# Kernel tuning notes

Hardware: AMD Instinct MI355X
Metric: run time of the kernel (lower is better)

Reference implementation:

```python
import jax, jax.numpy as jnp
import numpy as np

B = 8192
D = 512          # hidden_dim
OBS_EMB = 256
COMM = 128
N_ACT = 4
N_LAYERS = 2
D_INNER = 2 * D
D_STATE = 16
DT_RANK = D // 16  # 32
D_CONV = 4
EPS = 1e-5


def _xavier(k, shape):
    s = jnp.sqrt(2.0 / (shape[-2] + shape[-1]))
    return jax.random.normal(k, shape, jnp.float32) * s


def setup_inputs() -> dict:
    ks = jax.random.split(jax.random.key(0), 16)
    p = {}
    p['obs'] = jax.random.normal(ks[0], (B, 75), jnp.float32)
    p['comm_in'] = jax.random.normal(ks[1], (B, COMM), jnp.float32)
    # obs encoder: Conv2d(3->32, k=3, valid) + Linear(288->256)
    p['conv_w'] = jax.random.normal(ks[2], (32, 3, 3, 3), jnp.float32) * jnp.sqrt(2.0 / 27.0)
    p['conv_b'] = jnp.zeros((32,), jnp.float32)
    p['enc_w'] = _xavier(ks[3], (288, OBS_EMB))
    p['enc_b'] = jnp.zeros((OBS_EMB,), jnp.float32)
    p['proj_w'] = _xavier(ks[4], (OBS_EMB + COMM, D))
    p['proj_b'] = jnp.zeros((D,), jnp.float32)
    # Mamba stack params (stacked over layers)
    p['norm_w'] = jnp.ones((N_LAYERS, D), jnp.float32)
    p['in_proj_w'] = _xavier(ks[5], (N_LAYERS, D, 2 * D_INNER))
    p['conv1d_w'] = jax.random.normal(ks[6], (N_LAYERS, D_INNER, D_CONV), jnp.float32) / jnp.sqrt(D_CONV)
    p['conv1d_b'] = jnp.zeros((N_LAYERS, D_INNER), jnp.float32)
    p['x_proj_w'] = _xavier(ks[7], (N_LAYERS, D_INNER, DT_RANK + 2 * D_STATE))
    p['dt_proj_w'] = _xavier(ks[8], (N_LAYERS, DT_RANK, D_INNER))
    p['dt_proj_b'] = jnp.full((N_LAYERS, D_INNER), jnp.log(jnp.expm1(0.01)), jnp.float32)  # dt ~ 0.01
    p['A_log'] = jnp.log(jnp.broadcast_to(jnp.arange(1, D_STATE + 1, dtype=jnp.float32), (N_LAYERS, D_INNER, D_STATE)))
    p['D_param'] = jnp.ones((N_LAYERS, D_INNER), jnp.float32)
    p['out_proj_w'] = _xavier(ks[9], (N_LAYERS, D_INNER, D))
    p['final_norm_w'] = jnp.ones((D,), jnp.float32)
    # output heads
    p['act_w'] = _xavier(ks[10], (D, N_ACT)); p['act_b'] = jnp.zeros((N_ACT,), jnp.float32)
    p['comm_w'] = _xavier(ks[11], (D, COMM)); p['comm_b'] = jnp.zeros((COMM,), jnp.float32)
    p['val_w'] = _xavier(ks[12], (D, 1)); p['val_b'] = jnp.zeros((1,), jnp.float32)
    return p


def _rmsnorm(x, w):
    return x * jax.lax.rsqrt(jnp.mean(x * x, axis=-1, keepdims=True) + EPS) * w


def _mamba_block(u, Wi, cw, cb, Wx, Wdt, bdt, Alog, Dp, Wo):
    # u: (B, L, D) -> (B, L, D)
    Bsz, L, _ = u.shape
    d_inner = Dp.shape[0]
    x, z = jnp.split(u @ Wi, 2, axis=-1)                       # (B,L,di) each
    # causal depthwise conv1d over L
    xt = jnp.pad(jnp.swapaxes(x, 1, 2), ((0, 0), (0, 0), (D_CONV - 1, 0)))
    xc = jax.lax.conv_general_dilated(xt, cw[:, None, :], (1,), 'VALID',
                                      feature_group_count=d_inner,
                                      dimension_numbers=('NCH', 'OIH', 'NCH'))
    x = jax.nn.silu(jnp.swapaxes(xc, 1, 2) + cb)
    x_dbl = x @ Wx                                              # (B,L,dt_rank+2*ns)
    dt = jax.nn.softplus(x_dbl[..., :DT_RANK] @ Wdt + bdt)      # (B,L,di)
    Bm = x_dbl[..., DT_RANK:DT_RANK + D_STATE]                  # (B,L,ns)
    Cm = x_dbl[..., DT_RANK + D_STATE:]                         # (B,L,ns)
    A = -jnp.exp(Alog)                                          # (di,ns)
    dA = jnp.exp(dt[..., None] * A)                             # (B,L,di,ns)
    dBx = dt[..., None] * Bm[:, :, None, :] * x[..., None]      # (B,L,di,ns)

    def step(h, inp):
        dA_t, dBx_t, C_t = inp
        h = dA_t * h + dBx_t
        return h, jnp.einsum('bds,bs->bd', h, C_t)

    h0 = jnp.zeros((Bsz, d_inner, D_STATE), u.dtype)
    _, ys = jax.lax.scan(step, h0, (jnp.swapaxes(dA, 0, 1), jnp.swapaxes(dBx, 0, 1), jnp.swapaxes(Cm, 0, 1)))
    y = jnp.swapaxes(ys, 0, 1) + x * Dp
    return (y * jax.nn.silu(z)) @ Wo


def reference(obs, comm_in, conv_w, conv_b, enc_w, enc_b, proj_w, proj_b,
              norm_w, in_proj_w, conv1d_w, conv1d_b, x_proj_w, dt_proj_w, dt_proj_b,
              A_log, D_param, out_proj_w, final_norm_w,
              act_w, act_b, comm_w, comm_b, val_w, val_b):
    Bsz = obs.shape[0]
    v = obs.reshape(Bsz, 3, 5, 5)
    v = jax.lax.conv_general_dilated(v, conv_w, (1, 1), 'VALID',
                                     dimension_numbers=('NCHW', 'OIHW', 'NCHW'))
    v = jax.nn.relu(v + conv_b[None, :, None, None]).reshape(Bsz, -1)   # (B,288)
    emb = jax.nn.relu(v @ enc_w + enc_b)                                 # (B,256)
    x = jax.nn.relu(jnp.concatenate([emb, comm_in], axis=-1) @ proj_w + proj_b)  # (B,512)
    h = x[:, None, :]                                                    # (B, L=1, D)
    for i in range(norm_w.shape[0]):
        h = h + _mamba_block(_rmsnorm(h, norm_w[i]), in_proj_w[i], conv1d_w[i],
                             conv1d_b[i], x_proj_w[i], dt_proj_w[i], dt_proj_b[i],
                             A_log[i], D_param[i], out_proj_w[i])
    h = _rmsnorm(h, final_norm_w)[:, 0, :]
    action_logits = h @ act_w + act_b
    comm_out = jnp.tanh(h @ comm_w + comm_b)
    value = h @ val_w + val_b
    return action_logits, comm_out, value
```

## Files before the change

### kernel.cpp

```cpp
#include <hip/hip_runtime.h>
#include <math.h>


typedef __bf16 bf16x8 __attribute__((ext_vector_type(8)));
typedef float f32x4 __attribute__((ext_vector_type(4)));
typedef short short8 __attribute__((ext_vector_type(8)));

__device__ __forceinline__ float siluf(float v){ return v / (1.f + __expf(-v)); }
__device__ __forceinline__ float spfast(float v){ return v > 15.f ? v : __logf(1.f + __expf(v)); }
__device__ __forceinline__ float b2f(unsigned short u){ return __uint_as_float(((unsigned)u)<<16); }
__device__ __forceinline__ unsigned short f2b(float f){
  unsigned u = __float_as_uint(f);
  return (unsigned short)((u + 0x7fffu + ((u>>16)&1u)) >> 16);
}
__device__ __forceinline__ void g2l16(const void* g, void* l){
  __builtin_amdgcn_global_load_lds((const __attribute__((address_space(1))) unsigned int*)g,
                                   (__attribute__((address_space(3))) unsigned int*)l, 16, 0, 0);
}

__global__ __launch_bounds__(256) void k_wt_all(
    const float* __restrict__ in_proj_w, const float* __restrict__ out_proj_w,
    const float* __restrict__ x_proj_w,  const float* __restrict__ dt_proj_w,
    const float* __restrict__ enc_w,     const float* __restrict__ proj_w,
    const float* __restrict__ act_w, const float* __restrict__ comm_w, const float* __restrict__ val_w,
    unsigned short* __restrict__ wi_t, unsigned short* __restrict__ wo_t,
    unsigned short* __restrict__ wx_t, unsigned short* __restrict__ wdt_t,
    unsigned short* __restrict__ we_t, unsigned short* __restrict__ wp_t,
    unsigned short* __restrict__ wh_t)
{
  int b = blockIdx.x;
  if (b >= 3536) {
    const int n = b - 3536;
    for (int k = threadIdx.x; k < 512; k += 256) {
      float v;
      if (n < 4)         v = act_w[k*4 + n];
      else if (n < 132)  v = comm_w[k*128 + (n-4)];
      else if (n == 132) v = val_w[k];
      else               v = 0.f;
      wh_t[(size_t)n*512 + k] = f2b(v);
    }
    return;
  }
  const float* Wsrc; unsigned short* Wdst; int Kd, Nd, KP, nkb;
  if (b < 2048) {
    const int L = b >> 10; b &= 1023;
    Wsrc = in_proj_w + (size_t)L*512*2048; Wdst = wi_t + (size_t)L*2048*512;
    Kd = 512; Nd = 2048; KP = 512; nkb = 16;
  } else if (b < 3072) {
    b -= 2048; const int L = b >> 9; b &= 511;
    Wsrc = out_proj_w + (size_t)L*1024*512; Wdst = wo_t + (size_t)L*512*1024;
    Kd = 1024; Nd = 512; KP = 1024; nkb = 32;
  } else if (b < 3200) {
    b -= 3072; const int L = b >> 6; b &= 63;
    Wsrc = x_proj_w + (size_t)L*1024*64; Wdst = wx_t + (size_t)L*64*1024;
    Kd = 1024; Nd = 64; KP = 1024; nkb = 32;
  } else if (b < 3264) {
    b -= 3200; const int L = b >> 5; b &= 31;
    Wsrc = dt_proj_w + (size_t)L*32*1024; Wdst = wdt_t + (size_t)L*1024*32;
    Kd = 32; Nd = 1024; KP = 32; nkb = 1;
  } else if (b < 3344) {
    b -= 3264; Wsrc = enc_w; Wdst = we_t; Kd = 288; Nd = 256; KP = 320; nkb = 10;
  } else {
    b -= 3344; Wsrc = proj_w; Wdst = wp_t; Kd = 384; Nd = 512; KP = 384; nkb = 12;
  }
  __shared__ float s[32][33];
  const int kb = (b % nkb)*32, nb = (b / nkb)*32;
  const int c = threadIdx.x & 31, r = threadIdx.x >> 5;
  #pragma unroll
  for (int i=0;i<32;i+=8) {
    const int k = kb + r + i;
    s[r+i][c] = (k < Kd) ? Wsrc[(size_t)k*Nd + nb + c] : 0.f;
  }
  __syncthreads();
  #pragma unroll
  for (int i=0;i<32;i+=8) Wdst[(size_t)(nb+r+i)*KP + kb + c] = f2b(s[c][r+i]);
}

__global__ __launch_bounds__(256) void k_rms(const float* __restrict__ h,
                                             const float* __restrict__ nw,
                                             unsigned short* __restrict__ u)
{
  const int l = threadIdx.x & 63;
  const size_t row = (size_t)blockIdx.x*4 + (threadIdx.x>>6);
  const float4* hp = (const float4*)(h + row*512) + l*2;
  float4 v0 = hp[0], v1 = hp[1];
  float ss = v0.x*v0.x+v0.y*v0.y+v0.z*v0.z+v0.w*v0.w
           + v1.x*v1.x+v1.y*v1.y+v1.z*v1.z+v1.w*v1.w;
  #pragma unroll
  for (int m=32;m;m>>=1) ss += __shfl_xor(ss, m, 64);
  const float sc = rsqrtf(ss*(1.f/512.f) + 1e-5f);
  const float4* np = (const float4*)nw + l*2;
  float4 w0 = np[0], w1 = np[1];
  short8 o;
  o[0]=(short)f2b(v0.x*sc*w0.x); o[1]=(short)f2b(v0.y*sc*w0.y);
  o[2]=(short)f2b(v0.z*sc*w0.z); o[3]=(short)f2b(v0.w*sc*w0.w);
  o[4]=(short)f2b(v1.x*sc*w1.x); o[5]=(short)f2b(v1.y*sc*w1.y);
  o[6]=(short)f2b(v1.z*sc*w1.z); o[7]=(short)f2b(v1.w*sc*w1.w);
  *(short8*)(u + row*512 + l*8) = o;
}

template<int K>
__device__ __forceinline__ void gemm128(const unsigned short* __restrict__ A,
                                        const unsigned short* __restrict__ Bt,
                                        int r0, int c0,
                                        unsigned short* sA, unsigned short* sB,
                                        f32x4 acc[4][4])
{
  const int tid = threadIdx.x;
  const int l = tid & 63;
  const int wr = (tid>>7)&1, wc = (tid>>6)&1;
  const int rowA = tid>>3, kc8 = (tid&7)*8;
  const unsigned short* gA = A  + (size_t)(r0+rowA)*K + kc8;
  const unsigned short* gB = Bt + (size_t)(c0+rowA)*K + kc8;
  const int aOff = (wr*64 + (l&15))*64 + ((l>>4)*8);
  const int bOff = (wc*64 + (l&15))*64 + ((l>>4)*8);
  for (int kt=0; kt<K; kt+=64) {
    #pragma unroll
    for (int it=0; it<4; ++it) {
      g2l16(gA + (size_t)(it*32)*K + kt, sA + ((it*256+tid)*8));
      g2l16(gB + (size_t)(it*32)*K + kt, sB + ((it*256+tid)*8));
    }
    __syncthreads();
    #pragma unroll
    for (int ks=0; ks<64; ks+=32) {
      bf16x8 af[4], bfm[4];
      #pragma unroll
      for (int m=0;m<4;m++) af[m]  = *(const bf16x8*)(sA + (m*16)*64 + aOff + ks);
      #pragma unroll
      for (int n=0;n<4;n++) bfm[n] = *(const bf16x8*)(sB + (n*16)*64 + bOff + ks);
      #pragma unroll
      for (int m=0;m<4;m++)
        #pragma unroll
        for (int n=0;n<4;n++)
          acc[m][n] = __builtin_amdgcn_mfma_f32_16x16x32_bf16(af[m], bfm[n], acc[m][n], 0, 0, 0);
    }
    __syncthreads();
  }
}

__global__ __launch_bounds__(256) void k_gemm_inproj(
    const unsigned short* __restrict__ A, const unsigned short* __restrict__ Bt,
    const float* __restrict__ cw, const float* __restrict__ cb,
    unsigned short* __restrict__ xs, unsigned short* __restrict__ zs)
{
  __shared__ unsigned short sA[128*64], sB[128*64];
  f32x4 acc[4][4];
  #pragma unroll
  for (int m=0;m<4;m++)
    #pragma unroll
    for (int n=0;n<4;n++) acc[m][n] = (f32x4){0.f,0.f,0.f,0.f};
  const int r0 = blockIdx.x*128, c0 = blockIdx.y*128;
  gemm128<512>(A, Bt, r0, c0, sA, sB, acc);

  const int tid = threadIdx.x, l = tid & 63;
  const int wr = (tid>>7)&1, wc = (tid>>6)&1;
  const int colB = c0 + wc*64 + (l&15);
  const int rowB = r0 + wr*64 + ((l>>4)*4);
  if (c0 < 1024) {
    #pragma unroll
    for (int n=0;n<4;n++){
      const int col = colB + n*16;
      const float cw3 = cw[col*4+3], cbv = cb[col];
      #pragma unroll
      for (int m=0;m<4;m++)
        #pragma unroll
        for (int j=0;j<4;j++){
          const int row = rowB + m*16 + j;
          xs[(size_t)row*1024 + col] = f2b(siluf(fmaf(acc[m][n][j], cw3, cbv)));
        }
    }
  } else {
    #pragma unroll
    for (int n=0;n<4;n++){
      const int col = colB + n*16 - 1024;
      #pragma unroll
      for (int m=0;m<4;m++)
        #pragma unroll
        for (int j=0;j<4;j++){
          const int row = rowB + m*16 + j;
          zs[(size_t)row*1024 + col] = f2b(siluf(acc[m][n][j]));
        }
    }
  }
}

__global__ __launch_bounds__(256) void k_gemm_outproj(
    const unsigned short* __restrict__ A, const unsigned short* __restrict__ Bt,
    float* __restrict__ h)
{
  __shared__ unsigned short sA[128*64], sB[128*64];
  f32x4 acc[4][4];
  #pragma unroll
  for (int m=0;m<4;m++)
    #pragma unroll
    for (int n=0;n<4;n++) acc[m][n] = (f32x4){0.f,0.f,0.f,0.f};
  const int r0 = blockIdx.x*128, c0 = blockIdx.y*128;
  gemm128<1024>(A, Bt, r0, c0, sA, sB, acc);

  const int tid = threadIdx.x, l = tid & 63;
  const int wr = (tid>>7)&1, wc = (tid>>6)&1;
  const int colB = c0 + wc*64 + (l&15);
  const int rowB = r0 + wr*64 + ((l>>4)*4);
  #pragma unroll
  for (int n=0;n<4;n++){
    const int col = colB + n*16;
    #pragma unroll
    for (int m=0;m<4;m++)
      #pragma unroll
      for (int j=0;j<4;j++){
        const int row = rowB + m*16 + j;
        h[(size_t)row*512 + col] += acc[m][n][j];
      }
  }
}

__global__ __launch_bounds__(256) void k_gemm_enc(
    const unsigned short* __restrict__ A, const unsigned short* __restrict__ Bt,
    const float* __restrict__ bias, unsigned short* __restrict__ cat)
{
  __shared__ unsigned short sA[128*64], sB[128*64];
  f32x4 acc[4][4];
  #pragma unroll
  for (int m=0;m<4;m++)
    #pragma unroll
    for (int n=0;n<4;n++) acc[m][n] = (f32x4){0.f,0.f,0.f,0.f};
  const int r0 = blockIdx.x*128, c0 = blockIdx.y*128;
  gemm128<320>(A, Bt, r0, c0, sA, sB, acc);

  const int tid = threadIdx.x, l = tid & 63;
  const int wr = (tid>>7)&1, wc = (tid>>6)&1;
  const int colB = c0 + wc*64 + (l&15);
  const int rowB = r0 + wr*64 + ((l>>4)*4);
  #pragma unroll
  for (int n=0;n<4;n++){
    const int col = colB + n*16;
    const float bv = bias[col];
    #pragma unroll
    for (int m=0;m<4;m++)
      #pragma unroll
      for (int j=0;j<4;j++){
        const size_t row = rowB + m*16 + j;
        cat[row*384 + col] = f2b(fmaxf(acc[m][n][j] + bv, 0.f));
      }
  }
}

__global__ __launch_bounds__(256) void k_gemm_proj(
    const unsigned short* __restrict__ A, const unsigned short* __restrict__ Bt,
    const float* __restrict__ bias, float* __restrict__ h)
{
  __shared__ unsigned short sA[128*64], sB[128*64];
  f32x4 acc[4][4];
  #pragma unroll
  for (int m=0;m<4;m++)
    #pragma unroll
    for (int n=0;n<4;n++) acc[m][n] = (f32x4){0.f,0.f,0.f,0.f};
  const int r0 = blockIdx.x*128, c0 = blockIdx.y*128;
  gemm128<384>(A, Bt, r0, c0, sA, sB, acc);

  const int tid = threadIdx.x, l = tid & 63;
  const int wr = (tid>>7)&1, wc = (tid>>6)&1;
  const int colB = c0 + wc*64 + (l&15);
  const int rowB = r0 + wr*64 + ((l>>4)*4);
  #pragma unroll
  for (int n=0;n<4;n++){
    const int col = colB + n*16;
    const float bv = bias[col];
    #pragma unroll
    for (int m=0;m<4;m++)
      #pragma unroll
      for (int j=0;j<4;j++){
        const size_t row = rowB + m*16 + j;
        h[row*512 + col] = fmaxf(acc[m][n][j] + bv, 0.f);
      }
  }
}

__global__ __launch_bounds__(256) void k_front_prep(
    const float* __restrict__ obs, const float* __restrict__ comm_in,
    const float* __restrict__ conv_w, const float* __restrict__ conv_b,
    unsigned short* __restrict__ v, unsigned short* __restrict__ cat)
{
  __shared__ float s_obs[8][76];
  const int t = threadIdx.x;
  const int r0 = blockIdx.x * 8;

  for (int i = t; i < 8*75; i += 256) s_obs[i/75][i%75] = obs[(size_t)(r0 + i/75)*75 + i%75];
  __syncthreads();

  for (int i = t; i < 8*288; i += 256) {
    int r = i / 288, o = i % 288;
    int c = o / 9, ij = o % 9, oi = ij/3, oj = ij%3;
    float acc = conv_b[c];
    #pragma unroll
    for (int ic=0; ic<3; ic++)
      #pragma unroll
      for (int ki=0; ki<3; ki++)
        #pragma unroll
        for (int kj=0; kj<3; kj++)
          acc = fmaf(s_obs[r][ic*25 + (oi+ki)*5 + (oj+kj)], conv_w[((c*3+ic)*3+ki)*3+kj], acc);
    v[(size_t)(r0+r)*320 + o] = f2b(fmaxf(acc, 0.f));
  }
  v[(size_t)(r0 + (t>>5))*320 + 288 + (t&31)] = 0;
  for (int i = t; i < 8*128; i += 256) {
    int r = i >> 7, c = i & 127;
    cat[(size_t)(r0+r)*384 + 256 + c] = f2b(comm_in[(size_t)(r0+r)*128 + c]);
  }
}

__global__ __launch_bounds__(256) void k_gemm_heads(
    const unsigned short* __restrict__ A, const unsigned short* __restrict__ Bt,
    const float* __restrict__ act_b, const float* __restrict__ comm_b,
    const float* __restrict__ val_b, float* __restrict__ out)
{
  __shared__ unsigned short sA[128*64], sB[128*64];
  f32x4 acc[4][4];
  #pragma unroll
  for (int m=0;m<4;m++)
    #pragma unroll
    for (int n=0;n<4;n++) acc[m][n] = (f32x4){0.f,0.f,0.f,0.f};
  const int r0 = blockIdx.x*128, c0 = blockIdx.y*128;
  gemm128<512>(A, Bt, r0, c0, sA, sB, acc);

  const int tid = threadIdx.x, l = tid & 63;
  const int wr = (tid>>7)&1, wc = (tid>>6)&1;
  const int colB = c0 + wc*64 + (l&15);
  const int rowB = r0 + wr*64 + ((l>>4)*4);
  #pragma unroll
  for (int n=0;n<4;n++){
    const int col = colB + n*16;
    if (col > 132) continue;
    #pragma unroll
    for (int m=0;m<4;m++)
      #pragma unroll
      for (int j=0;j<4;j++){
        const size_t row = rowB + m*16 + j;
        float v = acc[m][n][j];
        if (col < 4)        out[row*4 + col] = v + act_b[col];
        else if (col < 132) out[32768 + row*128 + (col-4)] = tanhf(v + comm_b[col-4]);
        else                out[1081344 + row] = v + val_b[0];
      }
  }
}

__global__ __launch_bounds__(256) void k_xdbl(
    const unsigned short* __restrict__ A, const unsigned short* __restrict__ Bt,
    float* __restrict__ xdbl)
{
  __shared__ unsigned short sA[128*64], sB[64*64];
  f32x4 acc[2][4];
  #pragma unroll
  for (int m=0;m<2;m++)
    #pragma unroll
    for (int n=0;n<4;n++) acc[m][n] = (f32x4){0.f,0.f,0.f,0.f};
  const int tid = threadIdx.x, l = tid & 63, w = tid>>6;
  const int r0 = blockIdx.x*128;
  const int rowA = tid>>3, kc8 = (tid&7)*8;
  const unsigned short* gA = A  + (size_t)(r0+rowA)*1024 + kc8;
  const unsigned short* gB = Bt + (size_t)rowA*1024 + kc8;
  const int aOff = (w*32 + (l&15))*64 + ((l>>4)*8);
  const int bOff = ((l&15))*64 + ((l>>4)*8);
  for (int kt=0; kt<1024; kt+=64) {
    #pragma unroll
    for (int it=0; it<4; ++it) g2l16(gA + (size_t)(it*32)*1024 + kt, sA + (it*256+tid)*8);
    #pragma unroll
    for (int it=0; it<2; ++it) g2l16(gB + (size_t)(it*32)*1024 + kt, sB + (it*256+tid)*8);
    __syncthreads();
    #pragma unroll
    for (int ks=0; ks<64; ks+=32) {
      bf16x8 af[2], bfm[4];
      #pragma unroll
      for (int m=0;m<2;m++) af[m]  = *(const bf16x8*)(sA + (m*16)*64 + aOff + ks);
      #pragma unroll
      for (int n=0;n<4;n++) bfm[n] = *(const bf16x8*)(sB + (n*16)*64 + bOff + ks);
      #pragma unroll
      for (int m=0;m<2;m++)
        #pragma unroll
        for (int n=0;n<4;n++)
          acc[m][n] = __builtin_amdgcn_mfma_f32_16x16x32_bf16(af[m], bfm[n], acc[m][n], 0, 0, 0);
    }
    __syncthreads();
  }
  #pragma unroll
  for (int n=0;n<4;n++){
    const int col = n*16 + (l&15);
    #pragma unroll
    for (int m=0;m<2;m++)
      #pragma unroll
      for (int j=0;j<4;j++){
        const size_t row = r0 + w*32 + m*16 + (l>>4)*4 + j;
        xdbl[row*64 + col] = acc[m][n][j];
      }
  }
}

__global__ __launch_bounds__(256) void k_dtgate(
    unsigned short* __restrict__ xs, const unsigned short* __restrict__ zs,
    const float* __restrict__ xdbl, const unsigned short* __restrict__ Wdt_t,
    const float* __restrict__ bdt, const float* __restrict__ Dp)
{
  __shared__ unsigned short sA[128*32];
  __shared__ unsigned short sB[128*32];
  __shared__ float s_bc[128];
  const int tid = threadIdx.x, l = tid & 63;
  const int r0 = blockIdx.x*128, c0 = blockIdx.y*128;

  {
    const int row = tid >> 1, kh = (tid & 1)*16;
    const float4* p = (const float4*)(xdbl + (size_t)(r0+row)*64 + kh);
    float4 a = p[0], b = p[1], c = p[2], d = p[3];
    short8 o0, o1;
    o0[0]=(short)f2b(a.x); o0[1]=(short)f2b(a.y); o0[2]=(short)f2b(a.z); o0[3]=(short)f2b(a.w);
    o0[4]=(short)f2b(b.x); o0[5]=(short)f2b(b.y); o0[6]=(short)f2b(b.z); o0[7]=(short)f2b(b.w);
    o1[0]=(short)f2b(c.x); o1[1]=(short)f2b(c.y); o1[2]=(short)f2b(c.z); o1[3]=(short)f2b(c.w);
    o1[4]=(short)f2b(d.x); o1[5]=(short)f2b(d.y); o1[6]=(short)f2b(d.z); o1[7]=(short)f2b(d.w);
    *(short8*)(sA + row*32 + kh)     = o0;
    *(short8*)(sA + row*32 + kh + 8) = o1;
  }
  {
    const int nrow = tid >> 1, kh = (tid & 1)*16;
    const short8* wp = (const short8*)(Wdt_t + (size_t)(c0+nrow)*32 + kh);
    *(short8*)(sB + nrow*32 + kh)     = wp[0];
    *(short8*)(sB + nrow*32 + kh + 8) = wp[1];
  }
  if (tid < 128) {
    const float4* q = (const float4*)(xdbl + (size_t)(r0+tid)*64 + 32);
    float4 b0=q[0], b1=q[1], b2=q[2], b3=q[3];
    float4 c0v=q[4], c1=q[5], c2=q[6], c3=q[7];
    float acc = b0.x*c0v.x + b0.y*c0v.y + b0.z*c0v.z + b0.w*c0v.w
              + b1.x*c1.x + b1.y*c1.y + b1.z*c1.z + b1.w*c1.w
              + b2.x*c2.x + b2.y*c2.y + b2.z*c2.z + b2.w*c2.w
              + b3.x*c3.x + b3.y*c3.y + b3.z*c3.z + b3.w*c3.w;
    s_bc[tid] = acc;
  }
  __syncthreads();

  const int wr = (tid>>7)&1, wc = (tid>>6)&1;
  bf16x8 af[4], bfm[4];
  #pragma unroll
  for (int m=0;m<4;m++) af[m]  = *(const bf16x8*)(sA + (wr*64 + m*16 + (l&15))*32 + (l>>4)*8);
  #pragma unroll
  for (int n=0;n<4;n++) bfm[n] = *(const bf16x8*)(sB + (wc*64 + n*16 + (l&15))*32 + (l>>4)*8);
  f32x4 acc[4][4];
  #pragma unroll
  for (int m=0;m<4;m++)
    #pragma unroll
    for (int n=0;n<4;n++)
      acc[m][n] = __builtin_amdgcn_mfma_f32_16x16x32_bf16(af[m], bfm[n], (f32x4){0.f,0.f,0.f,0.f}, 0, 0, 0);

  #pragma unroll
  for (int n=0;n<4;n++){
    const int col = c0 + wc*64 + n*16 + (l&15);
    const float bj = bdt[col], dpj = Dp[col];
    #pragma unroll
    for (int m=0;m<4;m++){
      const int rloc = wr*64 + m*16 + (l>>4)*4;
      #pragma unroll
      for (int j=0;j<4;j++){
        const size_t row = r0 + rloc + j;
        const float dtv = spfast(acc[m][n][j] + bj);
        const float f = fmaf(dtv, s_bc[rloc + j], dpj);
        const float x = b2f(xs[row*1024 + col]);
        const float z = b2f(zs[row*1024 + col]);
        xs[row*1024 + col] = f2b(x * f * z);
      }
    }
  }
}

extern "C" void kernel_launch(void* const* d_in, const int* in_sizes, int n_in,
                              void* d_out, int out_size, void* d_ws, size_t ws_size,
                              hipStream_t stream) {
  const float* obs       = (const float*)d_in[0];
  const float* comm_in   = (const float*)d_in[1];
  const float* conv_w    = (const float*)d_in[2];
  const float* conv_b    = (const float*)d_in[3];
  const float* enc_w     = (const float*)d_in[4];
  const float* enc_b     = (const float*)d_in[5];
  const float* proj_w    = (const float*)d_in[6];
  const float* proj_b    = (const float*)d_in[7];
  const float* norm_w    = (const float*)d_in[8];
  const float* in_proj_w = (const float*)d_in[9];
  const float* conv1d_w  = (const float*)d_in[10];
  const float* conv1d_b  = (const float*)d_in[11];
  const float* x_proj_w  = (const float*)d_in[12];
  const float* dt_proj_w = (const float*)d_in[13];
  const float* dt_proj_b = (const float*)d_in[14];
  const float* D_param   = (const float*)d_in[16];
  const float* out_proj_w= (const float*)d_in[17];
  const float* final_nw  = (const float*)d_in[18];
  const float* act_w     = (const float*)d_in[19];
  const float* act_b     = (const float*)d_in[20];
  const float* comm_w    = (const float*)d_in[21];
  const float* comm_b    = (const float*)d_in[22];
  const float* val_w     = (const float*)d_in[23];
  const float* val_b     = (const float*)d_in[24];
  float* out = (float*)d_out;

  char* W = (char*)d_ws;
  float* h             = (float*)W;
  unsigned short* u_b  = (unsigned short*)(W + (16u<<20));
  unsigned short* xs_b = (unsigned short*)(W + (24u<<20));
  unsigned short* zs_b = (unsigned short*)(W + (40u<<20));
  unsigned short* wi_t = (unsigned short*)(W + (56u<<20));
  unsigned short* wo_t = (unsigned short*)(W + (60u<<20));
  float* xdbl          = (float*)(W + (62u<<20));
  unsigned short* wx_t = (unsigned short*)(W + (64u<<20));
  unsigned short* wdt_t= (unsigned short*)(W + (64u<<20) + (256u<<10));
  unsigned short* wh_t = (unsigned short*)(W + (65u<<20));
  unsigned short* we_t = (unsigned short*)(W + (65u<<20) + (512u<<10));
  unsigned short* wp_t = (unsigned short*)(W + (66u<<20));

  unsigned short* v_b   = xs_b;
  unsigned short* cat_b = zs_b;

  k_wt_all<<<3792,256,0,stream>>>(in_proj_w, out_proj_w, x_proj_w, dt_proj_w,
                                  enc_w, proj_w, act_w, comm_w, val_w,
                                  wi_t, wo_t, wx_t, wdt_t, we_t, wp_t, wh_t);

  k_front_prep<<<1024,256,0,stream>>>(obs, comm_in, conv_w, conv_b, v_b, cat_b);
  k_gemm_enc<<<dim3(64,2),256,0,stream>>>(v_b, we_t, enc_b, cat_b);
  k_gemm_proj<<<dim3(64,4),256,0,stream>>>(cat_b, wp_t, proj_b, h);

  for (int L=0; L<2; L++) {
    k_rms<<<2048,256,0,stream>>>(h, norm_w + L*512, u_b);
    k_gemm_inproj<<<dim3(64,16),256,0,stream>>>(u_b, wi_t + (size_t)L*2048*512,
                                                conv1d_w + L*1024*4, conv1d_b + L*1024, xs_b, zs_b);
    k_xdbl<<<64,256,0,stream>>>(xs_b, wx_t + (size_t)L*64*1024, xdbl);
    k_dtgate<<<dim3(64,8),256,0,stream>>>(xs_b, zs_b, xdbl, wdt_t + (size_t)L*1024*32,
                                          dt_proj_b + L*1024, D_param + L*1024);
    k_gemm_outproj<<<dim3(64,4),256,0,stream>>>(xs_b, wo_t + (size_t)L*512*1024, h);
  }
  k_rms<<<2048,256,0,stream>>>(h, final_nw, u_b);
  k_gemm_heads<<<dim3(64,2),256,0,stream>>>(u_b, wh_t, act_b, comm_b, val_b, out);
}
```

Baseline: 279.4 us.

## Narrow GEMM tiles, split x_proj finer with precomputed dt/BC, merge front prep

The small-N GEMMs (enc, proj, out_proj, heads) move to 128x64 tiles to launch more blocks on the 256-CU device. The x_proj GEMM now runs with 32-row blocks (256 blocks instead of 64) and directly writes bf16 dt inputs and the B·C dot product, so dtgate no longer converts or reduces xdbl. The front-end conv preprocessing is folded into the weight-transpose launch to save one kernel launch. Narrower tiles reduce A-tile reuse and add redundant A loads.

After: 253.7 us. 9.2% less time.

```diff
diff --git a/kernel.cpp b/kernel.cpp
--- a/kernel.cpp
+++ b/kernel.cpp
@@ -5,6 +5,7 @@
 typedef __bf16 bf16x8 __attribute__((ext_vector_type(8)));
 typedef float f32x4 __attribute__((ext_vector_type(4)));
 typedef short short8 __attribute__((ext_vector_type(8)));
+typedef short short4v __attribute__((ext_vector_type(4)));
 
 __device__ __forceinline__ float siluf(float v){ return v / (1.f + __expf(-v)); }
 __device__ __forceinline__ float spfast(float v){ return v > 15.f ? v : __logf(1.f + __expf(v)); }
@@ -23,21 +24,51 @@
     const float* __restrict__ x_proj_w,  const float* __restrict__ dt_proj_w,
     const float* __restrict__ enc_w,     const float* __restrict__ proj_w,
     const float* __restrict__ act_w, const float* __restrict__ comm_w, const float* __restrict__ val_w,
+    const float* __restrict__ obs, const float* __restrict__ comm_in,
+    const float* __restrict__ conv_w, const float* __restrict__ conv_b,
     unsigned short* __restrict__ wi_t, unsigned short* __restrict__ wo_t,
     unsigned short* __restrict__ wx_t, unsigned short* __restrict__ wdt_t,
     unsigned short* __restrict__ we_t, unsigned short* __restrict__ wp_t,
-    unsigned short* __restrict__ wh_t)
+    unsigned short* __restrict__ wh_t,
+    unsigned short* __restrict__ v, unsigned short* __restrict__ cat)
 {
   int b = blockIdx.x;
+  const int t = threadIdx.x;
+
+  if (b >= 3792) {
+    __shared__ float s_obs[8][76];
+    const int r0 = (b - 3792) * 8;
+    for (int i = t; i < 8*75; i += 256) s_obs[i/75][i%75] = obs[(size_t)(r0 + i/75)*75 + i%75];
+    __syncthreads();
+    for (int i = t; i < 8*288; i += 256) {
+      int r = i / 288, o = i % 288;
+      int c = o / 9, ij = o % 9, oi = ij/3, oj = ij%3;
+      float acc = conv_b[c];
+      #pragma unroll
+      for (int ic=0; ic<3; ic++)
+        #pragma unroll
+        for (int ki=0; ki<3; ki++)
+          #pragma unroll
+          for (int kj=0; kj<3; kj++)
+            acc = fmaf(s_obs[r][ic*25 + (oi+ki)*5 + (oj+kj)], conv_w[((c*3+ic)*3+ki)*3+kj], acc);
+      v[(size_t)(r0+r)*320 + o] = f2b(fmaxf(acc, 0.f));
+    }
+    v[(size_t)(r0 + (t>>5))*320 + 288 + (t&31)] = 0;
+    for (int i = t; i < 8*128; i += 256) {
+      int r = i >> 7, c = i & 127;
+      cat[(size_t)(r0+r)*384 + 256 + c] = f2b(comm_in[(size_t)(r0+r)*128 + c]);
+    }
+    return;
+  }
   if (b >= 3536) {
     const int n = b - 3536;
-    for (int k = threadIdx.x; k < 512; k += 256) {
-      float v;
-      if (n < 4)         v = act_w[k*4 + n];
-      else if (n < 132)  v = comm_w[k*128 + (n-4)];
-      else if (n == 132) v = val_w[k];
-      else               v = 0.f;
-      wh_t[(size_t)n*512 + k] = f2b(v);
+    for (int k = t; k < 512; k += 256) {
+      float v2;
+      if (n < 4)         v2 = act_w[k*4 + n];
+      else if (n < 132)  v2 = comm_w[k*128 + (n-4)];
+      else if (n == 132) v2 = val_w[k];
+      else               v2 = 0.f;
+      wh_t[(size_t)n*512 + k] = f2b(v2);
     }
     return;
   }
@@ -65,7 +96,7 @@
   }
   __shared__ float s[32][33];
   const int kb = (b % nkb)*32, nb = (b / nkb)*32;
-  const int c = threadIdx.x & 31, r = threadIdx.x >> 5;
+  const int c = t & 31, r = t >> 5;
   #pragma unroll
   for (int i=0;i<32;i+=8) {
     const int k = kb + r + i;
@@ -99,13 +130,14 @@
   *(short8*)(u + row*512 + l*8) = o;
 }
 
-template<int K>
-__device__ __forceinline__ void gemm128(const unsigned short* __restrict__ A,
-                                        const unsigned short* __restrict__ Bt,
-                                        int r0, int c0,
-                                        unsigned short* sA, unsigned short* sB,
-                                        f32x4 acc[4][4])
-{
+template<int K, int NB>
+__device__ __forceinline__ void gemmT(const unsigned short* __restrict__ A,
+                                      const unsigned short* __restrict__ Bt,
+                                      int r0, int c0,
+                                      unsigned short* sA, unsigned short* sB,
+                                      f32x4 (&acc)[4][NB/32])
+{
+  constexpr int NF = NB/32;
   const int tid = threadIdx.x;
   const int l = tid & 63;
   const int wr = (tid>>7)&1, wc = (tid>>6)&1;
@@ -113,25 +145,24 @@
   const unsigned short* gA = A  + (size_t)(r0+rowA)*K + kc8;
   const unsigned short* gB = Bt + (size_t)(c0+rowA)*K + kc8;
   const int aOff = (wr*64 + (l&15))*64 + ((l>>4)*8);
-  const int bOff = (wc*64 + (l&15))*64 + ((l>>4)*8);
+  const int bOff = (wc*(NB/2) + (l&15))*64 + ((l>>4)*8);
   for (int kt=0; kt<K; kt+=64) {
     #pragma unroll
-    for (int it=0; it<4; ++it) {
-      g2l16(gA + (size_t)(it*32)*K + kt, sA + ((it*256+tid)*8));
-      g2l16(gB + (size_t)(it*32)*K + kt, sB + ((it*256+tid)*8));
-    }
+    for (int it=0; it<4; ++it) g2l16(gA + (size_t)(it*32)*K + kt, sA + ((it*256+tid)*8));
+    #pragma unroll
+    for (int it=0; it<NB/32; ++it) g2l16(gB + (size_t)(it*32)*K + kt, sB + ((it*256+tid)*8));
     __syncthreads();
     #pragma unroll
     for (int ks=0; ks<64; ks+=32) {
-      bf16x8 af[4], bfm[4];
+      bf16x8 af[4], bfm[NF];
       #pragma unroll
       for (int m=0;m<4;m++) af[m]  = *(const bf16x8*)(sA + (m*16)*64 + aOff + ks);
       #pragma unroll
-      for (int n=0;n<4;n++) bfm[n] = *(const bf16x8*)(sB + (n*16)*64 + bOff + ks);
+      for (int n=0;n<NF;n++) bfm[n] = *(const bf16x8*)(sB + (n*16)*64 + bOff + ks);
       #pragma unroll
       for (int m=0;m<4;m++)
         #pragma unroll
-        for (int n=0;n<4;n++)
+        for (int n=0;n<NF;n++)
           acc[m][n] = __builtin_amdgcn_mfma_f32_16x16x32_bf16(af[m], bfm[n], acc[m][n], 0, 0, 0);
     }
     __syncthreads();
@@ -150,7 +181,7 @@
     #pragma unroll
     for (int n=0;n<4;n++) acc[m][n] = (f32x4){0.f,0.f,0.f,0.f};
   const int r0 = blockIdx.x*128, c0 = blockIdx.y*128;
-  gemm128<512>(A, Bt, r0, c0, sA, sB, acc);
+  gemmT<512,128>(A, Bt, r0, c0, sA, sB, acc);
 
   const int tid = threadIdx.x, l = tid & 63;
   const int wr = (tid>>7)&1, wc = (tid>>6)&1;
@@ -188,21 +219,21 @@
     const unsigned short* __restrict__ A, const unsigned short* __restrict__ Bt,
     float* __restrict__ h)
 {
-  __shared__ unsigned short sA[128*64], sB[128*64];
-  f32x4 acc[4][4];
+  __shared__ unsigned short sA[128*64], sB[64*64];
+  f32x4 acc[4][2];
   #pragma unroll
   for (int m=0;m<4;m++)
     #pragma unroll
-    for (int n=0;n<4;n++) acc[m][n] = (f32x4){0.f,0.f,0.f,0.f};
-  const int r0 = blockIdx.x*128, c0 = blockIdx.y*128;
-  gemm128<1024>(A, Bt, r0, c0, sA, sB, acc);
+    for (int n=0;n<2;n++) acc[m][n] = (f32x4){0.f,0.f,0.f,0.f};
+  const int r0 = blockIdx.x*128, c0 = blockIdx.y*64;
+  gemmT<1024,64>(A, Bt, r0, c0, sA, sB, acc);
 
   const int tid = threadIdx.x, l = tid & 63;
   const int wr = (tid>>7)&1, wc = (tid>>6)&1;
-  const int colB = c0 + wc*64 + (l&15);
+  const int colB = c0 + wc*32 + (l&15);
   const int rowB = r0 + wr*64 + ((l>>4)*4);
   #pragma unroll
-  for (int n=0;n<4;n++){
+  for (int n=0;n<2;n++){
     const int col = colB + n*16;
     #pragma unroll
     for (int m=0;m<4;m++)
@@ -218,21 +249,21 @@
     const unsigned short* __restrict__ A, const unsigned short* __restrict__ Bt,
     const float* __restrict__ bias, unsigned short* __restrict__ cat)
 {
-  __shared__ unsigned short sA[128*64], sB[128*64];
-  f32x4 acc[4][4];
+  __shared__ unsigned short sA[128*64], sB[64*64];
+  f32x4 acc[4][2];
   #pragma unroll
   for (int m=0;m<4;m++)
     #pragma unroll
-    for (int n=0;n<4;n++) acc[m][n] = (f32x4){0.f,0.f,0.f,0.f};
-  const int r0 = blockIdx.x*128, c0 = blockIdx.y*128;
-  gemm128<320>(A, Bt, r0, c0, sA, sB, acc);
+    for (int n=0;n<2;n++) acc[m][n] = (f32x4){0.f,0.f,0.f,0.f};
+  const int r0 = blockIdx.x*128, c0 = blockIdx.y*64;
+  gemmT<320,64>(A, Bt, r0, c0, sA, sB, acc);
 
   const int tid = threadIdx.x, l = tid & 63;
   const int wr = (tid>>7)&1, wc = (tid>>6)&1;
-  const int colB = c0 + wc*64 + (l&15);
+  const int colB = c0 + wc*32 + (l&15);
   const int rowB = r0 + wr*64 + ((l>>4)*4);
   #pragma unroll
-  for (int n=0;n<4;n++){
+  for (int n=0;n<2;n++){
     const int col = colB + n*16;
     const float bv = bias[col];
     #pragma unroll
@@ -249,21 +280,21 @@
     const unsigned short* __restrict__ A, const unsigned short* __restrict__ Bt,
     const float* __restrict__ bias, float* __restrict__ h)
 {
-  __shared__ unsigned short sA[128*64], sB[128*64];
-  f32x4 acc[4][4];
+  __shared__ unsigned short sA[128*64], sB[64*64];
+  f32x4 acc[4][2];
   #pragma unroll
   for (int m=0;m<4;m++)
     #pragma unroll
-    for (int n=0;n<4;n++) acc[m][n] = (f32x4){0.f,0.f,0.f,0.f};
-  const int r0 = blockIdx.x*128, c0 = blockIdx.y*128;
-  gemm128<384>(A, Bt, r0, c0, sA, sB, acc);
+    for (int n=0;n<2;n++) acc[m][n] = (f32x4){0.f,0.f,0.f,0.f};
+  const int r0 = blockIdx.x*128, c0 = blockIdx.y*64;
+  gemmT<384,64>(A, Bt, r0, c0, sA, sB, acc);
 
   const int tid = threadIdx.x, l = tid & 63;
   const int wr = (tid>>7)&1, wc = (tid>>6)&1;
-  const int colB = c0 + wc*64 + (l&15);
+  const int colB = c0 + wc*32 + (l&15);
   const int rowB = r0 + wr*64 + ((l>>4)*4);
   #pragma unroll
-  for (int n=0;n<4;n++){
+  for (int n=0;n<2;n++){
     const int col = colB + n*16;
     const float bv = bias[col];
     #pragma unroll
@@ -276,58 +307,26 @@
   }
 }
 
-__global__ __launch_bounds__(256) void k_front_prep(
-    const float* __restrict__ obs, const float* __restrict__ comm_in,
-    const float* __restrict__ conv_w, const float* __restrict__ conv_b,
-    unsigned short* __restrict__ v, unsigned short* __restrict__ cat)
-{
-  __shared__ float s_obs[8][76];
-  const int t = threadIdx.x;
-  const int r0 = blockIdx.x * 8;
-
-  for (int i = t; i < 8*75; i += 256) s_obs[i/75][i%75] = obs[(size_t)(r0 + i/75)*75 + i%75];
-  __syncthreads();
-
-  for (int i = t; i < 8*288; i += 256) {
-    int r = i / 288, o = i % 288;
-    int c = o / 9, ij = o % 9, oi = ij/3, oj = ij%3;
-    float acc = conv_b[c];
-    #pragma unroll
-    for (int ic=0; ic<3; ic++)
-      #pragma unroll
-      for (int ki=0; ki<3; ki++)
-        #pragma unroll
-        for (int kj=0; kj<3; kj++)
-          acc = fmaf(s_obs[r][ic*25 + (oi+ki)*5 + (oj+kj)], conv_w[((c*3+ic)*3+ki)*3+kj], acc);
-    v[(size_t)(r0+r)*320 + o] = f2b(fmaxf(acc, 0.f));
-  }
-  v[(size_t)(r0 + (t>>5))*320 + 288 + (t&31)] = 0;
-  for (int i = t; i < 8*128; i += 256) {
-    int r = i >> 7, c = i & 127;
-    cat[(size_t)(r0+r)*384 + 256 + c] = f2b(comm_in[(size_t)(r0+r)*128 + c]);
-  }
-}
-
 __global__ __launch_bounds__(256) void k_gemm_heads(
     const unsigned short* __restrict__ A, const unsigned short* __restrict__ Bt,
     const float* __restrict__ act_b, const float* __restrict__ comm_b,
     const float* __restrict__ val_b, float* __restrict__ out)
 {
-  __shared__ unsigned short sA[128*64], sB[128*64];
-  f32x4 acc[4][4];
+  __shared__ unsigned short sA[128*64], sB[64*64];
+  f32x4 acc[4][2];
   #pragma unroll
   for (int m=0;m<4;m++)
     #pragma unroll
-    for (int n=0;n<4;n++) acc[m][n] = (f32x4){0.f,0.f,0.f,0.f};
-  const int r0 = blockIdx.x*128, c0 = blockIdx.y*128;
-  gemm128<512>(A, Bt, r0, c0, sA, sB, acc);
+    for (int n=0;n<2;n++) acc[m][n] = (f32x4){0.f,0.f,0.f,0.f};
+  const int r0 = blockIdx.x*128, c0 = blockIdx.y*64;
+  gemmT<512,64>(A, Bt, r0, c0, sA, sB, acc);
 
   const int tid = threadIdx.x, l = tid & 63;
   const int wr = (tid>>7)&1, wc = (tid>>6)&1;
-  const int colB = c0 + wc*64 + (l&15);
+  const int colB = c0 + wc*32 + (l&15);
   const int rowB = r0 + wr*64 + ((l>>4)*4);
   #pragma unroll
-  for (int n=0;n<4;n++){
+  for (int n=0;n<2;n++){
     const int col = colB + n*16;
     if (col > 132) continue;
     #pragma unroll
@@ -343,60 +342,63 @@
   }
 }
 
-__global__ __launch_bounds__(256) void k_xdbl(
-    const unsigned short* __restrict__ A, const unsigned short* __restrict__ Bt,
-    float* __restrict__ xdbl)
-{
-  __shared__ unsigned short sA[128*64], sB[64*64];
-  f32x4 acc[2][4];
-  #pragma unroll
-  for (int m=0;m<2;m++)
-    #pragma unroll
-    for (int n=0;n<4;n++) acc[m][n] = (f32x4){0.f,0.f,0.f,0.f};
-  const int tid = threadIdx.x, l = tid & 63, w = tid>>6;
-  const int r0 = blockIdx.x*128;
-  const int rowA = tid>>3, kc8 = (tid&7)*8;
-  const unsigned short* gA = A  + (size_t)(r0+rowA)*1024 + kc8;
-  const unsigned short* gB = Bt + (size_t)rowA*1024 + kc8;
-  const int aOff = (w*32 + (l&15))*64 + ((l>>4)*8);
-  const int bOff = ((l&15))*64 + ((l>>4)*8);
-  for (int kt=0; kt<1024; kt+=64) {
-    #pragma unroll
-    for (int it=0; it<4; ++it) g2l16(gA + (size_t)(it*32)*1024 + kt, sA + (it*256+tid)*8);
-    #pragma unroll
-    for (int it=0; it<2; ++it) g2l16(gB + (size_t)(it*32)*1024 + kt, sB + (it*256+tid)*8);
+__global__ __launch_bounds__(256) void k_xdbl2(
+    const unsigned short* __restrict__ xs, const unsigned short* __restrict__ Wx_t,
+    unsigned short* __restrict__ dt_in, float* __restrict__ bc_g)
+{
+  __shared__ unsigned short sA[32*128];
+  __shared__ unsigned short sB[64*128];
+  __shared__ float s_dbl[32][64];
+  const int tid = threadIdx.x, l = tid & 63, w = tid >> 6;
+  const int r0 = blockIdx.x * 32;
+  f32x4 acc0 = (f32x4){0.f,0.f,0.f,0.f}, acc1 = (f32x4){0.f,0.f,0.f,0.f};
+  for (int kt = 0; kt < 1024; kt += 128) {
+    #pragma unroll
+    for (int it=0; it<2; ++it) {
+      const int idx = it*256 + tid;
+      g2l16(xs + (size_t)(r0 + (idx>>4))*1024 + (idx&15)*8 + kt, sA + idx*8);
+    }
+    #pragma unroll
+    for (int it=0; it<4; ++it) {
+      const int idx = it*256 + tid;
+      g2l16(Wx_t + (size_t)(idx>>4)*1024 + (idx&15)*8 + kt, sB + idx*8);
+    }
     __syncthreads();
     #pragma unroll
-    for (int ks=0; ks<64; ks+=32) {
-      bf16x8 af[2], bfm[4];
-      #pragma unroll
-      for (int m=0;m<2;m++) af[m]  = *(const bf16x8*)(sA + (m*16)*64 + aOff + ks);
-      #pragma unroll
-      for (int n=0;n<4;n++) bfm[n] = *(const bf16x8*)(sB + (n*16)*64 + bOff + ks);
-      #pragma unroll
-      for (int m=0;m<2;m++)
-        #pragma unroll
-        for (int n=0;n<4;n++)
-          acc[m][n] = __builtin_amdgcn_mfma_f32_16x16x32_bf16(af[m], bfm[n], acc[m][n], 0, 0, 0);
+    for (int ks=0; ks<128; ks+=32) {
+      bf16x8 a0 = *(const bf16x8*)(sA + ((l&15))*128      + (l>>4)*8 + ks);
+      bf16x8 a1 = *(const bf16x8*)(sA + (16+(l&15))*128   + (l>>4)*8 + ks);
+      bf16x8 bf = *(const bf16x8*)(sB + (w*16+(l&15))*128 + (l>>4)*8 + ks);
+      acc0 = __builtin_amdgcn_mfma_f32_16x16x32_bf16(a0, bf, acc0, 0, 0, 0);
+      acc1 = __builtin_amdgcn_mfma_f32_16x16x32_bf16(a1, bf, acc1, 0, 0, 0);
     }
     __syncthreads();
   }
   #pragma unroll
-  for (int n=0;n<4;n++){
-    const int col = n*16 + (l&15);
-    #pragma unroll
-    for (int m=0;m<2;m++)
-      #pragma unroll
-      for (int j=0;j<4;j++){
-        const size_t row = r0 + w*32 + m*16 + (l>>4)*4 + j;
-        xdbl[row*64 + col] = acc[m][n][j];
-      }
-  }
-}
-
-__global__ __launch_bounds__(256) void k_dtgate(
+  for (int j=0;j<4;j++) {
+    s_dbl[(l>>4)*4 + j]     [w*16 + (l&15)] = acc0[j];
+    s_dbl[16 + (l>>4)*4 + j][w*16 + (l&15)] = acc1[j];
+  }
+  __syncthreads();
+  if (tid < 32) {
+    float a = 0.f;
+    #pragma unroll
+    for (int s=0;s<16;s++) a = fmaf(s_dbl[tid][32+s], s_dbl[tid][48+s], a);
+    bc_g[r0 + tid] = a;
+  }
+  {
+    const int r = tid >> 3, c4 = (tid & 7)*4;
+    short4v o;
+    o[0] = (short)f2b(s_dbl[r][c4]);   o[1] = (short)f2b(s_dbl[r][c4+1]);
+    o[2] = (short)f2b(s_dbl[r][c4+2]); o[3] = (short)f2b(s_dbl[r][c4+3]);
+    *(short4v*)(dt_in + (size_t)(r0+r)*32 + c4) = o;
+  }
+}
+
+__global__ __launch_bounds__(256) void k_dtgate2(
     unsigned short* __restrict__ xs, const unsigned short* __restrict__ zs,
-    const float* __restrict__ xdbl, const unsigned short* __restrict__ Wdt_t,
+    const unsigned short* __restrict__ dt_in, const float* __restrict__ bc_g,
+    const unsigned short* __restrict__ Wdt_t,
     const float* __restrict__ bdt, const float* __restrict__ Dp)
 {
   __shared__ unsigned short sA[128*32];
@@ -405,34 +407,15 @@
   const int tid = threadIdx.x, l = tid & 63;
   const int r0 = blockIdx.x*128, c0 = blockIdx.y*128;
 
-  {
-    const int row = tid >> 1, kh = (tid & 1)*16;
-    const float4* p = (const float4*)(xdbl + (size_t)(r0+row)*64 + kh);
-    float4 a = p[0], b = p[1], c = p[2], d = p[3];
-    short8 o0, o1;
-    o0[0]=(short)f2b(a.x); o0[1]=(short)f2b(a.y); o0[2]=(short)f2b(a.z); o0[3]=(short)f2b(a.w);
-    o0[4]=(short)f2b(b.x); o0[5]=(short)f2b(b.y); o0[6]=(short)f2b(b.z); o0[7]=(short)f2b(b.w);
-    o1[0]=(short)f2b(c.x); o1[1]=(short)f2b(c.y); o1[2]=(short)f2b(c.z); o1[3]=(short)f2b(c.w);
-    o1[4]=(short)f2b(d.x); o1[5]=(short)f2b(d.y); o1[6]=(short)f2b(d.z); o1[7]=(short)f2b(d.w);
-    *(short8*)(sA + row*32 + kh)     = o0;
-    *(short8*)(sA + row*32 + kh + 8) = o1;
-  }
-  {
-    const int nrow = tid >> 1, kh = (tid & 1)*16;
-    const short8* wp = (const short8*)(Wdt_t + (size_t)(c0+nrow)*32 + kh);
-    *(short8*)(sB + nrow*32 + kh)     = wp[0];
-    *(short8*)(sB + nrow*32 + kh + 8) = wp[1];
-  }
-  if (tid < 128) {
-    const float4* q = (const float4*)(xdbl + (size_t)(r0+tid)*64 + 32);
-    float4 b0=q[0], b1=q[1], b2=q[2], b3=q[3];
-    float4 c0v=q[4], c1=q[5], c2=q[6], c3=q[7];
-    float acc = b0.x*c0v.x + b0.y*c0v.y + b0.z*c0v.z + b0.w*c0v.w
-              + b1.x*c1.x + b1.y*c1.y + b1.z*c1.z + b1.w*c1.w
-              + b2.x*c2.x + b2.y*c2.y + b2.z*c2.z + b2.w*c2.w
-              + b3.x*c3.x + b3.y*c3.y + b3.z*c3.z + b3.w*c3.w;
-    s_bc[tid] = acc;
-  }
+  { const int row = tid >> 1, kh = (tid & 1)*16;
+    const short8* ap = (const short8*)(dt_in + (size_t)(r0+row)*32 + kh);
+    *(short8*)(sA + row*32 + kh)     = ap[0];
+    *(short8*)(sA + row*32 + kh + 8) = ap[1];
+    const short8* wp = (const short8*)(Wdt_t + (size_t)(c0+row)*32 + kh);
+    *(short8*)(sB + row*32 + kh)     = wp[0];
+    *(short8*)(sB + row*32 + kh + 8) = wp[1];
+  }
+  if (tid < 128) s_bc[tid] = bc_g[r0 + tid];
   __syncthreads();
 
   const int wr = (tid>>7)&1, wc = (tid>>6)&1;
@@ -504,7 +487,8 @@
   unsigned short* zs_b = (unsigned short*)(W + (40u<<20));
   unsigned short* wi_t = (unsigned short*)(W + (56u<<20));
   unsigned short* wo_t = (unsigned short*)(W + (60u<<20));
-  float* xdbl          = (float*)(W + (62u<<20));
+  unsigned short* dt_in= (unsigned short*)(W + (62u<<20));
+  float* bc_g          = (float*)(W + (62u<<20) + (512u<<10));
   unsigned short* wx_t = (unsigned short*)(W + (64u<<20));
   unsigned short* wdt_t= (unsigned short*)(W + (64u<<20) + (256u<<10));
   unsigned short* wh_t = (unsigned short*)(W + (65u<<20));
@@ -514,23 +498,24 @@
   unsigned short* v_b   = xs_b;
   unsigned short* cat_b = zs_b;
 
-  k_wt_all<<<3792,256,0,stream>>>(in_proj_w, out_proj_w, x_proj_w, dt_proj_w,
+  k_wt_all<<<4816,256,0,stream>>>(in_proj_w, out_proj_w, x_proj_w, dt_proj_w,
                                   enc_w, proj_w, act_w, comm_w, val_w,
-                                  wi_t, wo_t, wx_t, wdt_t, we_t, wp_t, wh_t);
-
-  k_front_prep<<<1024,256,0,stream>>>(obs, comm_in, conv_w, conv_b, v_b, cat_b);
-  k_gemm_enc<<<dim3(64,2),256,0,stream>>>(v_b, we_t, enc_b, cat_b);
-  k_gemm_proj<<<dim3(64,4),256,0,stream>>>(cat_b, wp_t, proj_b, h);
+                                  obs, comm_in, conv_w, conv_b,
+                                  wi_t, wo_t, wx_t, wdt_t, we_t, wp_t, wh_t,
+                                  v_b, cat_b);
+
+  k_gemm_enc<<<dim3(64,4),256,0,stream>>>(v_b, we_t, enc_b, cat_b);
+  k_gemm_proj<<<dim3(64,8),256,0,stream>>>(cat_b, wp_t, proj_b, h);
 
   for (int L=0; L<2; L++) {
     k_rms<<<2048,256,0,stream>>>(h, norm_w + L*512, u_b);
     k_gemm_inproj<<<dim3(64,16),256,0,stream>>>(u_b, wi_t + (size_t)L*2048*512,
                                                 conv1d_w + L*1024*4, conv1d_b + L*1024, xs_b, zs_b);
-    k_xdbl<<<64,256,0,stream>>>(xs_b, wx_t + (size_t)L*64*1024, xdbl);
-    k_dtgate<<<dim3(64,8),256,0,stream>>>(xs_b, zs_b, xdbl, wdt_t + (size_t)L*1024*32,
-                                          dt_proj_b + L*1024, D_param + L*1024);
-    k_gemm_outproj<<<dim3(64,4),256,0,stream>>>(xs_b, wo_t + (size_t)L*512*1024, h);
+    k_xdbl2<<<256,256,0,stream>>>(xs_b, wx_t + (size_t)L*64*1024, dt_in, bc_g);
+    k_dtgate2<<<dim3(64,8),256,0,stream>>>(xs_b, zs_b, dt_in, bc_g, wdt_t + (size_t)L*1024*32,
+                                           dt_proj_b + L*1024, D_param + L*1024);
+    k_gemm_outproj<<<dim3(64,8),256,0,stream>>>(xs_b, wo_t + (size_t)L*512*1024, h);
   }
   k_rms<<<2048,256,0,stream>>>(h, final_nw, u_b);
-  k_gemm_heads<<<dim3(64,2),256,0,stream>>>(u_b, wh_t, act_b, comm_b, val_b, out);
-}
+  k_gemm_heads<<<dim3(64,4),256,0,stream>>>(u_b, wh_t, act_b, comm_b, val_b, out);
+}
```
